# Kernel optimization log

Hardware: AMD Instinct MI355X
Metric: run time of the kernel (lower is better)

Reference implementation:

```python
import jax, jax.numpy as jnp
import numpy as np

N_RES = 20000
N_EDGE = 640000
NUM_RBF = 16
NUM_POS = 16
NUM_AA = 21  # 20 + 1 (unknown)
D_MIN, D_MAX = 2.0, 22.0
EPS = 1e-8


def _quat_to_rot(q):
    # q = (w, x, y, z), assumed normalized
    w, x, y, z = q[..., 0], q[..., 1], q[..., 2], q[..., 3]
    r0 = jnp.stack([1 - 2 * (y * y + z * z), 2 * (x * y - w * z), 2 * (x * z + w * y)], -1)
    r1 = jnp.stack([2 * (x * y + w * z), 1 - 2 * (x * x + z * z), 2 * (y * z - w * x)], -1)
    r2 = jnp.stack([2 * (x * z - w * y), 2 * (y * z + w * x), 1 - 2 * (x * x + y * y)], -1)
    return jnp.stack([r0, r1, r2], -2)  # (..., 3, 3)


def _ideal_virtual_cb(bb):
    # bb: (N, 3, 3) with atoms N, CA, C
    n, ca, c = bb[..., 0, :], bb[..., 1, :], bb[..., 2, :]
    b = ca - n
    cc = c - ca
    a = jnp.cross(b, cc)
    return -0.58273431 * a + 0.56802827 * b - 0.54067466 * cc + ca


def _rbf(D):
    mu = jnp.linspace(D_MIN, D_MAX, NUM_RBF)  # (16,)
    sigma = (D_MAX - D_MIN) / NUM_RBF
    return jnp.exp(-(((D[..., None] - mu) / sigma) ** 2))


def setup_inputs() -> dict:
    key = jax.random.key(0)
    k1, k2, k3, k4, k5, k6 = jax.random.split(key, 6)
    atom14 = jax.random.normal(k1, (N_RES, 14, 3), jnp.float32) * 3.0
    quat = jax.random.normal(k2, (N_RES, 4), jnp.float32)
    quat = quat / jnp.linalg.norm(quat, axis=-1, keepdims=True)
    trans = jax.random.normal(k3, (N_RES, 3), jnp.float32) * 3.0
    rigids7 = jnp.concatenate([quat, trans], axis=-1)  # (N, 7)
    seq = jax.random.randint(k4, (N_RES,), 0, NUM_AA).astype(jnp.int32)
    noising_mask = jax.random.bernoulli(k5, 0.5, (N_RES,))
    edge_index = jax.random.randint(k6, (2, N_EDGE), 0, N_RES)
    return dict(atom14=atom14, rigids7=rigids7, seq=seq,
                noising_mask=noising_mask, edge_index=edge_index)


def reference(atom14, rigids7, seq, noising_mask, edge_index):
    dst, src = edge_index[0], edge_index[1]
    noised_src = noising_mask[src]
    noised_dst = noising_mask[dst]
    keep_src = (~noised_src)[:, None].astype(jnp.float32)
    keep_dst = (~noised_dst)[:, None].astype(jnp.float32)

    feats = [noised_dst.astype(jnp.float32)[:, None],
             noised_src.astype(jnp.float32)[:, None]]

    src_seq = jax.nn.one_hot(seq[src], NUM_AA, dtype=jnp.float32)
    dst_seq = jax.nn.one_hot(seq[dst], NUM_AA, dtype=jnp.float32)
    feats += [src_seq * keep_src, dst_seq * keep_dst]

    bb3 = atom14[:, :3, :]                      # N, CA, C
    cb = _ideal_virtual_cb(bb3)
    bb = jnp.concatenate([bb3, cb[:, None, :]], axis=1)  # (N, 4, 3)

    edge_bb_src = bb[src]                       # (E, 4, 3)
    edge_bb_dst = bb[dst]                       # (E, 4, 3)
    # pairwise distances between 4 backbone atoms of src and dst: (E, 4, 4)
    dists = jnp.linalg.norm(
        edge_bb_src[:, :, None, :] - edge_bb_dst[:, None, :, :] + EPS, axis=-1)
    feats.append(_rbf(dists).reshape(dists.shape[0], -1))  # (E, 256)

    # positional embedding of sequence separation
    d = (dst - src).astype(jnp.float32)
    freq = jnp.exp(jnp.arange(0, NUM_POS, 2, dtype=jnp.float32)
                   * (-np.log(10000.0) / NUM_POS))
    angles = d[:, None] * freq
    feats.append(jnp.concatenate([jnp.cos(angles), jnp.sin(angles)], axis=-1))

    # rigid frames: quaternion + translation; invert_apply = R^T (p - t)
    quat = rigids7[:, :4]
    quat = quat / jnp.linalg.norm(quat, axis=-1, keepdims=True)
    R = _quat_to_rot(quat)                      # (N, 3, 3)
    t = rigids7[:, 4:]                          # (N, 3)

    local = jnp.einsum('nji,nkj->nki', R, bb - t[:, None, :])  # (N, 4, 3)
    src_bb_local = local[src].reshape(-1, 12)

    Rs, ts = R[src], t[src]
    dst_in_src = jnp.einsum('eji,ekj->eki', Rs,
                            edge_bb_dst - ts[:, None, :]).reshape(-1, 12)

    feats += [src_bb_local * keep_src, dst_in_src * keep_dst]
    return jnp.concatenate(feats, axis=-1)  # (E, 340)
```

## Files before the change

kernel.cpp:

```cpp
#include <hip/hip_runtime.h>
#include <hip/hip_bf16.h>

#define N_RES   20000
#define N_EDGE  640000
#define NFEAT   340

__device__ __constant__ float c_freq[8] = {
    1.0f, 0.31622776601683794f, 0.1f, 0.031622776601683794f,
    0.01f, 0.0031622776601683794f, 0.001f, 0.00031622776601683794f};

extern "C" __global__ __launch_bounds__(256)
void residue_prep(const float* __restrict__ atom14,
                  const float* __restrict__ rigids7,
                  float* __restrict__ res) {
    int r = blockIdx.x * 256 + threadIdx.x;
    if (r >= N_RES) return;

    const float* a = atom14 + (size_t)r * 42;
    float nx  = a[0], ny  = a[1], nz  = a[2];
    float cax = a[3], cay = a[4], caz = a[5];
    float cx  = a[6], cy  = a[7], cz  = a[8];

    float bx = cax - nx, by = cay - ny, bz = caz - nz;
    float ex = cx - cax, ey = cy - cay, ez = cz - caz;
    float ax = by * ez - bz * ey;
    float ay = bz * ex - bx * ez;
    float az = bx * ey - by * ex;
    float cbx = -0.58273431f * ax + 0.56802827f * bx - 0.54067466f * ex + cax;
    float cby = -0.58273431f * ay + 0.56802827f * by - 0.54067466f * ey + cay;
    float cbz = -0.58273431f * az + 0.56802827f * bz - 0.54067466f * ez + caz;

    const float* q7 = rigids7 + (size_t)r * 7;
    float qw = q7[0], qx = q7[1], qy = q7[2], qz = q7[3];
    float inv = 1.0f / sqrtf(qw * qw + qx * qx + qy * qy + qz * qz);
    qw *= inv; qx *= inv; qy *= inv; qz *= inv;
    float tx = q7[4], ty = q7[5], tz = q7[6];

    float R[9];
    R[0] = 1.0f - 2.0f * (qy * qy + qz * qz);
    R[1] = 2.0f * (qx * qy - qw * qz);
    R[2] = 2.0f * (qx * qz + qw * qy);
    R[3] = 2.0f * (qx * qy + qw * qz);
    R[4] = 1.0f - 2.0f * (qx * qx + qz * qz);
    R[5] = 2.0f * (qy * qz - qw * qx);
    R[6] = 2.0f * (qx * qz - qw * qy);
    R[7] = 2.0f * (qy * qz + qw * qx);
    R[8] = 1.0f - 2.0f * (qx * qx + qy * qy);

    float bb[12] = {nx, ny, nz, cax, cay, caz, cx, cy, cz, cbx, cby, cbz};

    float* o = res + (size_t)r * 36;
    #pragma unroll
    for (int k = 0; k < 12; ++k) o[k] = bb[k];
    #pragma unroll
    for (int k = 0; k < 4; ++k) {
        float x0 = bb[k * 3 + 0] - tx;
        float x1 = bb[k * 3 + 1] - ty;
        float x2 = bb[k * 3 + 2] - tz;
        #pragma unroll
        for (int i = 0; i < 3; ++i)
            o[12 + k * 3 + i] = R[i] * x0 + R[3 + i] * x1 + R[6 + i] * x2;
    }
    #pragma unroll
    for (int j = 0; j < 9; ++j) o[24 + j] = R[j];
    o[33] = tx; o[34] = ty; o[35] = tz;
}

extern "C" __global__ __launch_bounds__(256)
void edge_feats(const int* __restrict__ eidx,
                const int* __restrict__ seq,
                const int* __restrict__ mask,
                const float* __restrict__ res,
                float* __restrict__ out) {
    int lane = threadIdx.x & 63;
    int wave = threadIdx.x >> 6;
    int e = blockIdx.x * 4 + wave;

    int dst = eidx[e];
    int src = eidx[N_EDGE + e];
    int msrc = mask[src];
    int mdst = mask[dst];
    float noised_src = msrc ? 1.0f : 0.0f;
    float noised_dst = mdst ? 1.0f : 0.0f;
    float keep_src = 1.0f - noised_src;
    float keep_dst = 1.0f - noised_dst;
    int ssrc = seq[src];
    int sdst = seq[dst];

    const float* rs = res + (size_t)src * 36;
    const float* rd = res + (size_t)dst * 36;

    int p  = lane & 15;
    int di = p >> 2;
    int dj = p & 3;
    float dx = rs[di * 3 + 0] - rd[dj * 3 + 0] + 1e-8f;
    float dy = rs[di * 3 + 1] - rd[dj * 3 + 1] + 1e-8f;
    float dz = rs[di * 3 + 2] - rd[dj * 3 + 2] + 1e-8f;
    float D = sqrtf(dx * dx + dy * dy + dz * dz);

    float dpos = (float)(dst - src);
    size_t base = (size_t)e * NFEAT;

    #pragma unroll
    for (int it = 0; it < 6; ++it) {
        int f = lane + it * 64;
        bool act = f < NFEAT;
        int q = f - 44;
        int srcLane = (q < 0) ? 0 : ((q >> 4) & 15);
        float Dq = __shfl(D, srcLane, 64);

        float v = 0.0f;
        if (act) {
            if (f < 2) {
                v = (f == 0) ? noised_dst : noised_src;
            } else if (f < 23) {
                v = (ssrc == f - 2) ? keep_src : 0.0f;
            } else if (f < 44) {
                v = (sdst == f - 23) ? keep_dst : 0.0f;
            } else if (f < 300) {
                int r = q & 15;
                float mu = 2.0f + (20.0f / 15.0f) * (float)r;
                float x = (Dq - mu) * 0.8f;
                v = __expf(-x * x);
            } else if (f < 316) {
                int m = f - 300;
                float ang = dpos * c_freq[m & 7];
                v = (m < 8) ? cosf(ang) : sinf(ang);
            } else if (f < 328) {
                v = rs[12 + (f - 316)] * keep_src;
            } else {
                int qq = f - 328;
                int k = qq / 3;
                int i = qq - k * 3;
                float x0 = rd[k * 3 + 0] - rs[33];
                float x1 = rd[k * 3 + 1] - rs[34];
                float x2 = rd[k * 3 + 2] - rs[35];
                v = (rs[24 + i] * x0 + rs[27 + i] * x1 + rs[30 + i] * x2) * keep_dst;
            }
            out[base + f] = v;
        }
    }
}

extern "C" void kernel_launch(void* const* d_in, const int* in_sizes, int n_in,
                              void* d_out, int out_size, void* d_ws, size_t ws_size,
                              hipStream_t stream) {
    const float* atom14  = (const float*)d_in[0];
    const float* rigids7 = (const float*)d_in[1];
    const int* seq  = (const int*)d_in[2];
    const int* mask = (const int*)d_in[3];
    const int* eidx = (const int*)d_in[4];
    float* res = (float*)d_ws;

    hipLaunchKernelGGL(residue_prep, dim3((N_RES + 255) / 256), dim3(256), 0, stream,
                       atom14, rigids7, res);
    hipLaunchKernelGGL(edge_feats, dim3(N_EDGE / 4), dim3(256), 0, stream,
                       eidx, seq, mask, res, (float*)d_out);
}
```

Baseline: 1.088 ms.

## Vectorize edge feature writes with float4 and precompute positional encoding table

Restructures the per-edge wave so each lane computes four RBF values and writes them with a single float4 store, and the other feature segments are split across dedicated lane groups instead of a 6-iteration branchy loop. The sinusoidal positional embedding is precomputed into a table indexed by sequence separation, so the trig calls leave the edge kernel. The edge index is also made wave-uniform via readfirstlane. This aims to cut store instruction count and divergent compute, at the cost of an extra small kernel and a gather from the table.

New measurement: 1.010 ms. 7.2% less time.

```diff
diff --git a/kernel.cpp b/kernel.cpp
--- a/kernel.cpp
+++ b/kernel.cpp
@@ -1,5 +1,4 @@
 #include <hip/hip_runtime.h>
-#include <hip/hip_bf16.h>
 
 #define N_RES   20000
 #define N_EDGE  640000
@@ -67,14 +66,25 @@
 }
 
 extern "C" __global__ __launch_bounds__(256)
+void pos_table(float* __restrict__ tab) {
+    int idx = blockIdx.x * 256 + threadIdx.x;
+    int row = idx >> 4;
+    int m = idx & 15;
+    float d = (float)(row - 19999);
+    float ang = d * c_freq[m & 7];
+    tab[idx] = (m < 8) ? cosf(ang) : sinf(ang);
+}
+
+extern "C" __global__ __launch_bounds__(256)
 void edge_feats(const int* __restrict__ eidx,
                 const int* __restrict__ seq,
                 const int* __restrict__ mask,
                 const float* __restrict__ res,
+                const float* __restrict__ postab,
                 float* __restrict__ out) {
     int lane = threadIdx.x & 63;
     int wave = threadIdx.x >> 6;
-    int e = blockIdx.x * 4 + wave;
+    int e = __builtin_amdgcn_readfirstlane((int)(blockIdx.x * 4 + wave));
 
     int dst = eidx[e];
     int src = eidx[N_EDGE + e];
@@ -89,56 +99,60 @@
 
     const float* rs = res + (size_t)src * 36;
     const float* rd = res + (size_t)dst * 36;
+    float* op = out + (size_t)e * NFEAT;
 
-    int p  = lane & 15;
-    int di = p >> 2;
-    int dj = p & 3;
-    float dx = rs[di * 3 + 0] - rd[dj * 3 + 0] + 1e-8f;
-    float dy = rs[di * 3 + 1] - rd[dj * 3 + 1] + 1e-8f;
-    float dz = rs[di * 3 + 2] - rd[dj * 3 + 2] + 1e-8f;
-    float D = sqrtf(dx * dx + dy * dy + dz * dz);
+    {
+        int ai = lane >> 4;
+        int aj = (lane >> 2) & 3;
+        const float* sp = rs + ai * 3;
+        const float* dp = rd + aj * 3;
+        float dx = sp[0] - dp[0] + 1e-8f;
+        float dy = sp[1] - dp[1] + 1e-8f;
+        float dz = sp[2] - dp[2] + 1e-8f;
+        float D = sqrtf(dx * dx + dy * dy + dz * dz);
 
-    float dpos = (float)(dst - src);
-    size_t base = (size_t)e * NFEAT;
+        int rbase = (lane & 3) * 4;
+        float4 v;
+        float x;
+        float mu;
+        mu = 2.0f + (20.0f / 15.0f) * (float)(rbase + 0);
+        x = (D - mu) * 0.8f;  v.x = __expf(-x * x);
+        mu = 2.0f + (20.0f / 15.0f) * (float)(rbase + 1);
+        x = (D - mu) * 0.8f;  v.y = __expf(-x * x);
+        mu = 2.0f + (20.0f / 15.0f) * (float)(rbase + 2);
+        x = (D - mu) * 0.8f;  v.z = __expf(-x * x);
+        mu = 2.0f + (20.0f / 15.0f) * (float)(rbase + 3);
+        x = (D - mu) * 0.8f;  v.w = __expf(-x * x);
 
-    #pragma unroll
-    for (int it = 0; it < 6; ++it) {
-        int f = lane + it * 64;
-        bool act = f < NFEAT;
-        int q = f - 44;
-        int srcLane = (q < 0) ? 0 : ((q >> 4) & 15);
-        float Dq = __shfl(D, srcLane, 64);
+        *reinterpret_cast<float4*>(op + 44 + 4 * lane) = v;
+    }
 
-        float v = 0.0f;
-        if (act) {
-            if (f < 2) {
-                v = (f == 0) ? noised_dst : noised_src;
-            } else if (f < 23) {
-                v = (ssrc == f - 2) ? keep_src : 0.0f;
-            } else if (f < 44) {
-                v = (sdst == f - 23) ? keep_dst : 0.0f;
-            } else if (f < 300) {
-                int r = q & 15;
-                float mu = 2.0f + (20.0f / 15.0f) * (float)r;
-                float x = (Dq - mu) * 0.8f;
-                v = __expf(-x * x);
-            } else if (f < 316) {
-                int m = f - 300;
-                float ang = dpos * c_freq[m & 7];
-                v = (m < 8) ? cosf(ang) : sinf(ang);
-            } else if (f < 328) {
-                v = rs[12 + (f - 316)] * keep_src;
-            } else {
-                int qq = f - 328;
-                int k = qq / 3;
-                int i = qq - k * 3;
-                float x0 = rd[k * 3 + 0] - rs[33];
-                float x1 = rd[k * 3 + 1] - rs[34];
-                float x2 = rd[k * 3 + 2] - rs[35];
-                v = (rs[24 + i] * x0 + rs[27 + i] * x1 + rs[30 + i] * x2) * keep_dst;
-            }
-            out[base + f] = v;
-        }
+    if (lane < 44) {
+        float v = (lane < 23) ? ((ssrc == lane - 2) ? keep_src : 0.0f)
+                              : ((sdst == lane - 23) ? keep_dst : 0.0f);
+        if (lane == 0) v = noised_dst;
+        if (lane == 1) v = noised_src;
+        op[lane] = v;
+    } else if (lane < 56) {
+        int qq = lane - 44;
+        int k = qq / 3;
+        int i2 = qq - k * 3;
+        float t0 = rs[33], t1 = rs[34], t2 = rs[35];
+        float x0 = rd[k * 3 + 0] - t0;
+        float x1 = rd[k * 3 + 1] - t1;
+        float x2 = rd[k * 3 + 2] - t2;
+        float v = (rs[24 + i2] * x0 + rs[27 + i2] * x1 + rs[30 + i2] * x2) * keep_dst;
+        op[328 + qq] = v;
+    } else if (lane < 60) {
+        int c = lane - 56;
+        const float4 v = *reinterpret_cast<const float4*>(
+            postab + ((size_t)(dst - src + 19999) * 16 + c * 4));
+        *reinterpret_cast<float4*>(op + 300 + 4 * c) = v;
+    } else if (lane < 63) {
+        int c = lane - 60;
+        float4 v = *reinterpret_cast<const float4*>(rs + 12 + 4 * c);
+        v.x *= keep_src; v.y *= keep_src; v.z *= keep_src; v.w *= keep_src;
+        *reinterpret_cast<float4*>(op + 316 + 4 * c) = v;
     }
 }
 
@@ -151,9 +165,11 @@
     const int* mask = (const int*)d_in[3];
     const int* eidx = (const int*)d_in[4];
     float* res = (float*)d_ws;
+    float* tab = res + 720000;
 
     hipLaunchKernelGGL(residue_prep, dim3((N_RES + 255) / 256), dim3(256), 0, stream,
                        atom14, rigids7, res);
+    hipLaunchKernelGGL(pos_table, dim3(2500), dim3(256), 0, stream, tab);
     hipLaunchKernelGGL(edge_feats, dim3(N_EDGE / 4), dim3(256), 0, stream,
-                       eidx, seq, mask, res, (float*)d_out);
+                       eidx, seq, mask, res, tab, (float*)d_out);
 }
```
